# Kernel optimization log

Hardware: AMD Instinct MI355X
Metric: run time of the kernel (lower is better)

## Reference

```python
import jax, jax.numpy as jnp
import numpy as np

B, T, D, H = 2, 2048, 1024, 16
HD = D // H
SCALE = HD ** -0.5


def setup_inputs() -> dict:
    key = jax.random.key(0)
    k1, k2, k3 = jax.random.split(key, 3)
    x = jax.random.normal(k1, (B, T, D), dtype=jnp.float32)
    w_qkv = jax.random.normal(k2, (D, 3 * D), dtype=jnp.float32) * (D ** -0.5)
    w_proj = jax.random.normal(k3, (D, D), dtype=jnp.float32) * (D ** -0.5)
    b_proj = jnp.zeros((D,), dtype=jnp.float32)
    return {"x": x, "w_qkv": w_qkv, "w_proj": w_proj, "b_proj": b_proj}


def reference(x, w_qkv, w_proj, b_proj):
    b, t, d = x.shape
    qkv = jnp.einsum('btd,de->bte', x, w_qkv)            # [B,T,3D]
    qkv = qkv.reshape(b, t, 3, H, HD)
    q = qkv[:, :, 0].transpose(0, 2, 1, 3)               # [B,H,T,HD]
    k = qkv[:, :, 1].transpose(0, 2, 1, 3)
    v = qkv[:, :, 2].transpose(0, 2, 1, 3)
    scores = jnp.einsum('bhqd,bhkd->bhqk', q, k) * SCALE  # [B,H,T,T]
    # NOTE: faithful to the source, softmax over dim=1 (the HEAD axis)
    probs = jax.nn.softmax(scores, axis=1)
    attn_out = jnp.einsum('bhqk,bhkd->bhqd', probs, v)
    attn_out = attn_out.transpose(0, 2, 1, 3).reshape(b, t, d)
    out = jnp.einsum('btd,de->bte', attn_out, w_proj) + b_proj
    return out
```

## Files before the change

kernel.cpp:

```cpp
#include <hip/hip_runtime.h>
#include <hip/hip_bf16.h>
#include <stdint.h>

typedef __bf16 bf16;
typedef __attribute__((ext_vector_type(8))) __bf16 bf16x8;
typedef __attribute__((ext_vector_type(4))) float f32x4;

#define MFMA_16x16x32(a, b, c) __builtin_amdgcn_mfma_f32_16x16x32_bf16((a), (b), (c), 0, 0, 0)

__device__ __forceinline__ void gld_lds16(const void* g, void* l) {
    __builtin_amdgcn_global_load_lds(
        (const __attribute__((address_space(1))) void*)g,
        (__attribute__((address_space(3))) void*)l,
        16, 0, 0);
}

__global__ void cvt_f32_bf16(const float* __restrict__ in, bf16* __restrict__ out, int n) {
    int i = (blockIdx.x * blockDim.x + threadIdx.x) * 8;
    if (i >= n) return;
    f32x4 a = *(const f32x4*)(in + i);
    f32x4 b = *(const f32x4*)(in + i + 4);
    bf16x8 o;
#pragma unroll
    for (int j = 0; j < 4; ++j) { o[j] = (bf16)a[j]; o[j + 4] = (bf16)b[j]; }
    *(bf16x8*)(out + i) = o;
}

__global__ void transpose_cvt(const float* __restrict__ in, bf16* __restrict__ out, int R, int C) {
    __shared__ float tile[32][33];
    int c0 = blockIdx.x * 32, r0 = blockIdx.y * 32;
    int tc = threadIdx.x & 31, tr = threadIdx.x >> 5;
#pragma unroll
    for (int i = 0; i < 4; ++i) {
        int r = tr + i * 8;
        tile[r][tc] = in[(size_t)(r0 + r) * C + c0 + tc];
    }
    __syncthreads();
#pragma unroll
    for (int i = 0; i < 4; ++i) {
        int r = tr + i * 8;
        out[(size_t)(c0 + r) * R + r0 + tc] = (bf16)tile[tc][r];
    }
}

template <int EPI>
__global__ void __launch_bounds__(256) gemm_bf16(
    const bf16* __restrict__ A, const bf16* __restrict__ Bt, int M, int N, int K,
    float* __restrict__ Cf, const float* __restrict__ bias,
    bf16* __restrict__ q_out, bf16* __restrict__ k_out, bf16* __restrict__ v_out)
{
    __shared__ bf16 As[128 * 32];
    __shared__ bf16 Bs[128 * 32];
    const int t = threadIdx.x, w = t >> 6, l = t & 63;
    const int l15 = l & 15, lh = l >> 4;
    const int m0 = blockIdx.y * 128, n0 = blockIdx.x * 128;
    const int wm = w >> 1, wn = w & 1;

    const int srow = w * 16 + (l >> 2);
    const int scol = (l & 3) * 8;
    const bf16* gA = A + (size_t)(m0 + srow) * K + scol;
    const bf16* gB = Bt + (size_t)(n0 + srow) * K + scol;
    char* lA = (char*)As + w * 1024;
    char* lB = (char*)Bs + w * 1024;

    f32x4 acc[4][4] = {};

    for (int kt = 0; kt < K; kt += 32) {
        __syncthreads();
        gld_lds16(gA + kt, lA);
        gld_lds16(gA + (size_t)64 * K + kt, lA + 4096);
        gld_lds16(gB + kt, lB);
        gld_lds16(gB + (size_t)64 * K + kt, lB + 4096);
        asm volatile("s_waitcnt vmcnt(0)" ::: "memory");
        __syncthreads();

        const bf16* pa = As + (wm * 64 + l15) * 32 + lh * 8;
        const bf16* pb = Bs + (wn * 64 + l15) * 32 + lh * 8;
        bf16x8 af[4], bfr[4];
#pragma unroll
        for (int i = 0; i < 4; ++i) {
            af[i]  = *(const bf16x8*)(pa + i * 512);
            bfr[i] = *(const bf16x8*)(pb + i * 512);
        }
#pragma unroll
        for (int mi = 0; mi < 4; ++mi)
#pragma unroll
            for (int ni = 0; ni < 4; ++ni)
                acc[mi][ni] = MFMA_16x16x32(af[mi], bfr[ni], acc[mi][ni]);
    }

    if (EPI == 1) {
#pragma unroll
        for (int ni = 0; ni < 4; ++ni) {
            int n = n0 + wn * 64 + ni * 16 + l15;
            float bb = bias[n];
#pragma unroll
            for (int mi = 0; mi < 4; ++mi)
#pragma unroll
                for (int r = 0; r < 4; ++r) {
                    int m = m0 + wm * 64 + mi * 16 + lh * 4 + r;
                    Cf[(size_t)m * N + n] = acc[mi][ni][r] + bb;
                }
        }
    } else {
        const int which = n0 >> 10;
#pragma unroll
        for (int ni = 0; ni < 4; ++ni) {
            int n = n0 + wn * 64 + ni * 16 + l15;
            int h = (n >> 6) & 15;
            int d = n & 63;
#pragma unroll
            for (int mi = 0; mi < 4; ++mi)
#pragma unroll
                for (int r = 0; r < 4; ++r) {
                    int m = m0 + wm * 64 + mi * 16 + lh * 4 + r;
                    int b = m >> 11, tt = m & 2047;
                    bf16 val = (bf16)acc[mi][ni][r];
                    size_t hb = (size_t)b * 16 + h;
                    if (which == 0)      q_out[(hb * 2048 + tt) * 64 + d] = val;
                    else if (which == 1) k_out[(hb * 2048 + tt) * 64 + d] = val;
                    else                 v_out[(hb * 64 + d) * 2048 + tt] = val;
                }
        }
    }
}

__global__ void __launch_bounds__(1024) attn_kernel(
    const bf16* __restrict__ Q, const bf16* __restrict__ Kmat, const bf16* __restrict__ Vt,
    bf16* __restrict__ part)
{
    __shared__ bf16 S[16][32][40];
    const int t = threadIdx.x;
    const int w = t >> 6;
    const int l = t & 63;
    const int l15 = l & 15, lh = l >> 4;

    const int bi = blockIdx.x;
    const int qtile = bi & 63;
    const int kslice = (bi >> 6) & 1;
    const int b = bi >> 7;
    const int qt = qtile * 32;

    const size_t headQK = ((size_t)b * 16 + w) * (2048 * 64);
    const size_t headV  = ((size_t)b * 16 + w) * (64 * 2048);

    bf16x8 aq[2][2];
#pragma unroll
    for (int qb2 = 0; qb2 < 2; ++qb2)
#pragma unroll
        for (int ds = 0; ds < 2; ++ds)
            aq[qb2][ds] = *(const bf16x8*)(Q + headQK + (size_t)(qt + qb2 * 16 + l15) * 64 + ds * 32 + lh * 8);

    f32x4 o[2][4] = {};
    const int qi = t >> 5, ki = t & 31;

    for (int it = 0; it < 32; ++it) {
        const int kt = kslice * 1024 + it * 32;
        __syncthreads();
#pragma unroll
        for (int kb = 0; kb < 2; ++kb) {
            const bf16* kp = Kmat + headQK + (size_t)(kt + kb * 16 + l15) * 64 + lh * 8;
            bf16x8 bk0 = *(const bf16x8*)(kp);
            bf16x8 bk1 = *(const bf16x8*)(kp + 32);
#pragma unroll
            for (int qb2 = 0; qb2 < 2; ++qb2) {
                f32x4 s = {};
                s = MFMA_16x16x32(aq[qb2][0], bk0, s);
                s = MFMA_16x16x32(aq[qb2][1], bk1, s);
#pragma unroll
                for (int r = 0; r < 4; ++r)
                    S[w][qb2 * 16 + lh * 4 + r][kb * 16 + l15] = (bf16)(s[r] * 0.125f);
            }
        }
        __syncthreads();
        {
            float sh[16];
            float mx = -1e30f;
#pragma unroll
            for (int hh = 0; hh < 16; ++hh) { sh[hh] = (float)S[hh][qi][ki]; mx = fmaxf(mx, sh[hh]); }
            float sum = 0.f;
#pragma unroll
            for (int hh = 0; hh < 16; ++hh) { float e = __expf(sh[hh] - mx); sh[hh] = e; sum += e; }
            float inv = 1.f / sum;
#pragma unroll
            for (int hh = 0; hh < 16; ++hh) S[hh][qi][ki] = (bf16)(sh[hh] * inv);
        }
        __syncthreads();
        bf16x8 bv[4];
#pragma unroll
        for (int ni = 0; ni < 4; ++ni)
            bv[ni] = *(const bf16x8*)(Vt + headV + (size_t)(ni * 16 + l15) * 2048 + kt + lh * 8);
#pragma unroll
        for (int qb2 = 0; qb2 < 2; ++qb2) {
            bf16x8 ap = *(const bf16x8*)(&S[w][qb2 * 16 + l15][lh * 8]);
#pragma unroll
            for (int ni = 0; ni < 4; ++ni)
                o[qb2][ni] = MFMA_16x16x32(ap, bv[ni], o[qb2][ni]);
        }
    }
    bf16* dst = part + (size_t)(kslice * 2 + b) * (2048 * 1024);
#pragma unroll
    for (int qb2 = 0; qb2 < 2; ++qb2)
#pragma unroll
        for (int ni = 0; ni < 4; ++ni)
#pragma unroll
            for (int r = 0; r < 4; ++r) {
                int tt = qt + qb2 * 16 + lh * 4 + r;
                int d = ni * 16 + l15;
                dst[(size_t)tt * 1024 + w * 64 + d] = (bf16)o[qb2][ni][r];
            }
}

__global__ void reduce_part(const bf16* __restrict__ part, bf16* __restrict__ out, int n) {
    int i = (blockIdx.x * blockDim.x + threadIdx.x) * 8;
    if (i >= n) return;
    bf16x8 a = *(const bf16x8*)(part + i);
    bf16x8 b = *(const bf16x8*)(part + n + i);
    bf16x8 o;
#pragma unroll
    for (int j = 0; j < 8; ++j) o[j] = (bf16)((float)a[j] + (float)b[j]);
    *(bf16x8*)(out + i) = o;
}

extern "C" void kernel_launch(void* const* d_in, const int* in_sizes, int n_in,
                              void* d_out, int out_size, void* d_ws, size_t ws_size,
                              hipStream_t stream)
{
    const float* x      = (const float*)d_in[0];
    const float* w_qkv  = (const float*)d_in[1];
    const float* w_proj = (const float*)d_in[2];
    const float* b_proj = (const float*)d_in[3];
    float* out = (float*)d_out;

    char* ws = (char*)d_ws;
    bf16* xb     = (bf16*)(ws + 0);
    bf16* wqkvT  = (bf16*)(ws + 8388608);
    bf16* wprojT = (bf16*)(ws + 14680064);
    bf16* qb     = (bf16*)(ws + 16777216);
    bf16* kb     = (bf16*)(ws + 25165824);
    bf16* vt     = (bf16*)(ws + 33554432);
    bf16* part   = (bf16*)(ws + 41943040);
    bf16* attnb  = (bf16*)(ws + 58720256);

    cvt_f32_bf16<<<2048, 256, 0, stream>>>(x, xb, 4194304);
    transpose_cvt<<<dim3(96, 32), 256, 0, stream>>>(w_qkv, wqkvT, 1024, 3072);
    transpose_cvt<<<dim3(32, 32), 256, 0, stream>>>(w_proj, wprojT, 1024, 1024);

    gemm_bf16<0><<<dim3(24, 32), 256, 0, stream>>>(xb, wqkvT, 4096, 3072, 1024,
                                                   nullptr, nullptr, qb, kb, vt);
    attn_kernel<<<256, 1024, 0, stream>>>(qb, kb, vt, part);
    reduce_part<<<2048, 256, 0, stream>>>(part, attnb, 4194304);
    gemm_bf16<1><<<dim3(8, 32), 256, 0, stream>>>(attnb, wprojT, 4096, 1024, 1024,
                                                  out, b_proj, nullptr, nullptr, nullptr);

    (void)in_sizes; (void)n_in; (void)out_size; (void)ws_size;
}
```

Baseline: 261.7 us.

## Split attention keys four ways and simplify head-axis softmax without max subtraction

The key dimension is now split into four slices instead of two, giving 512 blocks to improve occupancy. Each slice writes its own partial buffer, and these buffers reuse dead workspace regions. Softmax over heads drops the max subtraction: exp2 is applied to the scaled scores directly in the QK stage, and a reduced pass computes only per-(q,k) reciprocals of the head sums. The normalization multiply is folded into the PV operand load. This removes one exp pass and per-element max work, but risks overflow for large scores and adds a four-way partial reduction.

```diff
diff --git a/kernel.cpp b/kernel.cpp
--- a/kernel.cpp
+++ b/kernel.cpp
@@ -4,6 +4,7 @@
 
 typedef __bf16 bf16;
 typedef __attribute__((ext_vector_type(8))) __bf16 bf16x8;
+typedef __attribute__((ext_vector_type(2))) __bf16 bf16x2;
 typedef __attribute__((ext_vector_type(4))) float f32x4;
 
 #define MFMA_16x16x32(a, b, c) __builtin_amdgcn_mfma_f32_16x16x32_bf16((a), (b), (c), 0, 0, 0)
@@ -125,24 +126,25 @@
     }
 }
 
-__global__ void __launch_bounds__(1024) attn_kernel(
+__global__ void __launch_bounds__(1024, 8) attn_kernel(
     const bf16* __restrict__ Q, const bf16* __restrict__ Kmat, const bf16* __restrict__ Vt,
-    bf16* __restrict__ part)
+    bf16* __restrict__ p0, bf16* __restrict__ p1, bf16* __restrict__ p2, bf16* __restrict__ p3)
 {
     __shared__ bf16 S[16][32][40];
+    __shared__ bf16 invS[32][40];
     const int t = threadIdx.x;
     const int w = t >> 6;
     const int l = t & 63;
     const int l15 = l & 15, lh = l >> 4;
 
-    const int bi = blockIdx.x;
-    const int qtile = bi & 63;
-    const int kslice = (bi >> 6) & 1;
-    const int b = bi >> 7;
-    const int qt = qtile * 32;
+    const int bid = blockIdx.x;
+    const int b = (bid & 7) >> 2;
+    const int ks = bid & 3;
+    const int qt = (bid >> 3) * 32;
 
     const size_t headQK = ((size_t)b * 16 + w) * (2048 * 64);
     const size_t headV  = ((size_t)b * 16 + w) * (64 * 2048);
+    const float SCL = 0.125f * 1.44269504089f;
 
     bf16x8 aq[2][2];
 #pragma unroll
@@ -152,38 +154,43 @@
             aq[qb2][ds] = *(const bf16x8*)(Q + headQK + (size_t)(qt + qb2 * 16 + l15) * 64 + ds * 32 + lh * 8);
 
     f32x4 o[2][4] = {};
-    const int qi = t >> 5, ki = t & 31;
-
-    for (int it = 0; it < 32; ++it) {
-        const int kt = kslice * 1024 + it * 32;
-        __syncthreads();
+
+    for (int it = 0; it < 16; ++it) {
+        const int kt = ks * 512 + it * 32;
+        bf16x8 bk0[2], bk1[2];
 #pragma unroll
         for (int kb = 0; kb < 2; ++kb) {
             const bf16* kp = Kmat + headQK + (size_t)(kt + kb * 16 + l15) * 64 + lh * 8;
-            bf16x8 bk0 = *(const bf16x8*)(kp);
-            bf16x8 bk1 = *(const bf16x8*)(kp + 32);
+            bk0[kb] = *(const bf16x8*)(kp);
+            bk1[kb] = *(const bf16x8*)(kp + 32);
+        }
+        __syncthreads();
+#pragma unroll
+        for (int kb = 0; kb < 2; ++kb) {
 #pragma unroll
             for (int qb2 = 0; qb2 < 2; ++qb2) {
                 f32x4 s = {};
-                s = MFMA_16x16x32(aq[qb2][0], bk0, s);
-                s = MFMA_16x16x32(aq[qb2][1], bk1, s);
+                s = MFMA_16x16x32(aq[qb2][0], bk0[kb], s);
+                s = MFMA_16x16x32(aq[qb2][1], bk1[kb], s);
 #pragma unroll
                 for (int r = 0; r < 4; ++r)
-                    S[w][qb2 * 16 + lh * 4 + r][kb * 16 + l15] = (bf16)(s[r] * 0.125f);
+                    S[w][qb2 * 16 + lh * 4 + r][kb * 16 + l15] = (bf16)exp2f(s[r] * SCL);
             }
         }
         __syncthreads();
-        {
-            float sh[16];
-            float mx = -1e30f;
-#pragma unroll
-            for (int hh = 0; hh < 16; ++hh) { sh[hh] = (float)S[hh][qi][ki]; mx = fmaxf(mx, sh[hh]); }
-            float sum = 0.f;
-#pragma unroll
-            for (int hh = 0; hh < 16; ++hh) { float e = __expf(sh[hh] - mx); sh[hh] = e; sum += e; }
-            float inv = 1.f / sum;
-#pragma unroll
-            for (int hh = 0; hh < 16; ++hh) S[hh][qi][ki] = (bf16)(sh[hh] * inv);
+        if (t < 512) {
+            const int sqi = t >> 4, skc = (t & 15) * 2;
+            float s0 = 0.f, s1 = 0.f;
+#pragma unroll
+            for (int hh = 0; hh < 16; ++hh) {
+                bf16x2 pr = *(const bf16x2*)&S[hh][sqi][skc];
+                s0 += (float)pr[0];
+                s1 += (float)pr[1];
+            }
+            bf16x2 iv;
+            iv[0] = (bf16)__builtin_amdgcn_rcpf(s0);
+            iv[1] = (bf16)__builtin_amdgcn_rcpf(s1);
+            *(bf16x2*)&invS[sqi][skc] = iv;
         }
         __syncthreads();
         bf16x8 bv[4];
@@ -192,13 +199,18 @@
             bv[ni] = *(const bf16x8*)(Vt + headV + (size_t)(ni * 16 + l15) * 2048 + kt + lh * 8);
 #pragma unroll
         for (int qb2 = 0; qb2 < 2; ++qb2) {
-            bf16x8 ap = *(const bf16x8*)(&S[w][qb2 * 16 + l15][lh * 8]);
+            bf16x8 ev  = *(const bf16x8*)(&S[w][qb2 * 16 + l15][lh * 8]);
+            bf16x8 ivv = *(const bf16x8*)(&invS[qb2 * 16 + l15][lh * 8]);
+            bf16x8 ap;
+#pragma unroll
+            for (int j = 0; j < 8; ++j)
+                ap[j] = (bf16)((float)ev[j] * (float)ivv[j]);
 #pragma unroll
             for (int ni = 0; ni < 4; ++ni)
                 o[qb2][ni] = MFMA_16x16x32(ap, bv[ni], o[qb2][ni]);
         }
     }
-    bf16* dst = part + (size_t)(kslice * 2 + b) * (2048 * 1024);
+    bf16* dst = (ks == 0 ? p0 : ks == 1 ? p1 : ks == 2 ? p2 : p3) + (size_t)b * (2048 * 1024);
 #pragma unroll
     for (int qb2 = 0; qb2 < 2; ++qb2)
 #pragma unroll
@@ -211,14 +223,19 @@
             }
 }
 
-__global__ void reduce_part(const bf16* __restrict__ part, bf16* __restrict__ out, int n) {
+__global__ void reduce_part4(const bf16* __restrict__ p0, const bf16* __restrict__ p1,
+                             const bf16* __restrict__ p2, const bf16* __restrict__ p3,
+                             bf16* __restrict__ out, int n) {
     int i = (blockIdx.x * blockDim.x + threadIdx.x) * 8;
     if (i >= n) return;
-    bf16x8 a = *(const bf16x8*)(part + i);
-    bf16x8 b = *(const bf16x8*)(part + n + i);
+    bf16x8 a = *(const bf16x8*)(p0 + i);
+    bf16x8 b = *(const bf16x8*)(p1 + i);
+    bf16x8 c = *(const bf16x8*)(p2 + i);
+    bf16x8 d = *(const bf16x8*)(p3 + i);
     bf16x8 o;
 #pragma unroll
-    for (int j = 0; j < 8; ++j) o[j] = (bf16)((float)a[j] + (float)b[j]);
+    for (int j = 0; j < 8; ++j)
+        o[j] = (bf16)(((float)a[j] + (float)b[j]) + ((float)c[j] + (float)d[j]));
     *(bf16x8*)(out + i) = o;
 }
 
@@ -233,14 +250,18 @@
     float* out = (float*)d_out;
 
     char* ws = (char*)d_ws;
-    bf16* xb     = (bf16*)(ws + 0);
-    bf16* wqkvT  = (bf16*)(ws + 8388608);
-    bf16* wprojT = (bf16*)(ws + 14680064);
-    bf16* qb     = (bf16*)(ws + 16777216);
-    bf16* kb     = (bf16*)(ws + 25165824);
-    bf16* vt     = (bf16*)(ws + 33554432);
-    bf16* part   = (bf16*)(ws + 41943040);
-    bf16* attnb  = (bf16*)(ws + 58720256);
+    const size_t MB = 1048576;
+    bf16* wprojT = (bf16*)(ws + 0 * MB);
+    bf16* xb     = (bf16*)(ws + 2 * MB);
+    bf16* wqkvT  = (bf16*)(ws + 10 * MB);
+    bf16* qb     = (bf16*)(ws + 18 * MB);
+    bf16* kb     = (bf16*)(ws + 26 * MB);
+    bf16* vt     = (bf16*)(ws + 34 * MB);
+    bf16* part0  = (bf16*)(ws + 2 * MB);
+    bf16* part1  = (bf16*)(ws + 10 * MB);
+    bf16* part2  = (bf16*)(ws + 42 * MB);
+    bf16* part3  = (bf16*)(ws + 50 * MB);
+    bf16* attnb  = (bf16*)(ws + 2 * MB);
 
     cvt_f32_bf16<<<2048, 256, 0, stream>>>(x, xb, 4194304);
     transpose_cvt<<<dim3(96, 32), 256, 0, stream>>>(w_qkv, wqkvT, 1024, 3072);
@@ -248,8 +269,8 @@
 
     gemm_bf16<0><<<dim3(24, 32), 256, 0, stream>>>(xb, wqkvT, 4096, 3072, 1024,
                                                    nullptr, nullptr, qb, kb, vt);
-    attn_kernel<<<256, 1024, 0, stream>>>(qb, kb, vt, part);
-    reduce_part<<<2048, 256, 0, stream>>>(part, attnb, 4194304);
+    attn_kernel<<<512, 1024, 0, stream>>>(qb, kb, vt, part0, part1, part2, part3);
+    reduce_part4<<<2048, 256, 0, stream>>>(part0, part1, part2, part3, attnb, 4194304);
     gemm_bf16<1><<<dim3(8, 32), 256, 0, stream>>>(attnb, wprojT, 4096, 1024, 1024,
                                                   out, b_proj, nullptr, nullptr, nullptr);
 
```

After: 366.2 us. +39.9%, slower.
